# Kernel tuning notes

Measured on AMD Instinct MI355X. Metric: run time of the kernel, lower is better.

The kernel has to match this reference:

```python
import jax, jax.numpy as jnp
import numpy as np

K = 9            # kernel_size * dilation
ALPHA = 0.2      # LeakyReLU slope in GAT attention
LRELU = 0.01     # Grapher.layer1 default LeakyReLU slope
EPS_NORM = 1e-12
BN_EPS = 1e-5
NEG_INF = -9e15


def setup_inputs() -> dict:
    key = jax.random.key(0)
    ks = jax.random.split(key, 9)
    B, C, H, W = 16, 64, 32, 32
    nheads, nhid = 4, 15
    return {
        "x": jax.random.normal(ks[0], (B, C, H, W), jnp.float32),
        "W_heads": jax.random.normal(ks[1], (nheads, C, nhid), jnp.float32) * 0.2,
        "a_heads": jax.random.normal(ks[2], (nheads, 2 * nhid, 1), jnp.float32) * 0.2,
        "W_out": jax.random.normal(ks[3], (nheads * nhid, C), jnp.float32) * 0.2,
        "a_out": jax.random.normal(ks[4], (2 * C, 1), jnp.float32) * 0.2,
        "conv_w": jax.random.normal(ks[5], (C, C), jnp.float32) * 0.1,
        "conv_b": jax.random.normal(ks[6], (C,), jnp.float32) * 0.1,
        "bn_gamma": jnp.ones((C,), jnp.float32),
        "bn_beta": jnp.zeros((C,), jnp.float32),
    }


def _gat_layer(h, adj, W, a, concat):
    # h: [B,N,Fin], W: [Fin,Fout], a: [2*Fout,1]
    Wh = h @ W                                   # [B,N,Fout]
    Fout = W.shape[1]
    f1 = Wh @ a[:Fout]                           # [B,N,1]  (a . Wh_i)
    f2 = Wh @ a[Fout:]                           # [B,N,1]  (a . Wh_j)
    e = jax.nn.leaky_relu(f1 + jnp.swapaxes(f2, 1, 2), ALPHA)  # [B,N,N]
    att = jnp.where(adj > 0, e, NEG_INF)
    att = jax.nn.softmax(att, axis=1)            # torch F.softmax(dim=1)
    hp = att @ Wh                                # [B,N,Fout]
    return jax.nn.elu(hp) if concat else hp


def reference(x, W_heads, a_heads, W_out, a_out, conv_w, conv_b, bn_gamma, bn_beta):
    B, C, H, W = x.shape
    N = H * W
    res = x
    xf = x.reshape(B, C, N)                      # [B,C,N]
    # F.normalize(p=2, dim=1)
    nrm = jnp.maximum(jnp.linalg.norm(xf, axis=1, keepdims=True), EPS_NORM)
    h = jnp.swapaxes(xf / nrm, 1, 2)             # [B,N,C]
    # KNN adjacency (built under no_grad in the original)
    hs = jax.lax.stop_gradient(h)
    sq = jnp.sum(hs * hs, axis=-1, keepdims=True)        # [B,N,1]
    dist = sq - 2.0 * (hs @ jnp.swapaxes(hs, 1, 2)) + jnp.swapaxes(sq, 1, 2)
    _, idx = jax.lax.top_k(-dist, K)                      # [B,N,K]
    adj = jnp.zeros((B, N, N), x.dtype).at[
        jnp.arange(B)[:, None, None], jnp.arange(N)[None, :, None], idx
    ].set(1.0)
    # 4-head GAT (dropout is identity in eval mode)
    heads = [_gat_layer(h, adj, W_heads[i], a_heads[i], True)
             for i in range(W_heads.shape[0])]
    hcat = jnp.concatenate(heads, axis=2)        # [B,N,60]
    out = jax.nn.elu(_gat_layer(hcat, adj, W_out, a_out, False))  # [B,N,C]
    y = jnp.swapaxes(out, 1, 2).reshape(B, C, H, W)
    y = jax.nn.leaky_relu(y, LRELU)
    # 1x1 conv + BatchNorm (eval: running_mean=0, running_var=1)
    y = jnp.einsum('bchw,oc->bohw', y, conv_w) + conv_b[None, :, None, None]
    y = y / jnp.sqrt(1.0 + BN_EPS) * bn_gamma[None, :, None, None] + bn_beta[None, :, None, None]
    return y + res
```

## Files before the change

kernel.cpp:

```cpp
#include <hip/hip_runtime.h>
#include <math.h>

#define NB 16
#define NC 64
#define NN 1024
#define NK 9
#define NH 4
#define NF 15

#define OFF_HN     0
#define OFF_SQV    1048576
#define OFF_IDX    1064960
#define OFF_DEN1   1212416
#define OFF_U1     1277952
#define OFF_DEN2   1278976
#define OFF_U2     1295360
#define OFF_F11    1296384
#define OFF_F21    1361920
#define OFF_F12    1427456
#define OFF_F22    1443840
#define OFF_E1     1460224
#define OFF_E2     2050048
#define OFF_BIG    2197504
#define OFF_DIST   OFF_BIG
#define OFF_WH1    OFF_BIG
#define OFF_HCAT   3246080
#define OFF_WH2    4294656
#define OFF_YTIL   5343232
#define ZERO_BASE  OFF_DEN1
#define ZERO_LEN   83968

__device__ __forceinline__ unsigned fkey(float x){
  unsigned b = __float_as_uint(x);
  return (b & 0x80000000u) ? ~b : (b | 0x80000000u);
}
__device__ __forceinline__ float eluf(float x){ return x > 0.f ? x : expm1f(x); }

__global__ __launch_bounds__(256) void k1_norm(const float* __restrict__ x,
                                               float* __restrict__ hn, float* __restrict__ sqv,
                                               float* __restrict__ ws){
  int t = blockIdx.x*256 + threadIdx.x;
  if (t < ZERO_LEN) ws[ZERO_BASE + t] = 0.f;
  if (t >= NB*NN) return;
  int b = t >> 10, n = t & 1023;
  const float* xb = x + b*NC*NN;
  float* hb = hn + b*NC*NN;
  float s = 0.f;
  #pragma unroll
  for (int c = 0; c < NC; c++){ float v = xb[c*NN + n]; s = fmaf(v, v, s); }
  float nrm = fmaxf(sqrtf(s), 1e-12f);
  float s2 = 0.f;
  #pragma unroll
  for (int c = 0; c < NC; c++){
    float v = xb[c*NN + n] / nrm;
    hb[c*NN + n] = v;
    s2 = fmaf(v, v, s2);
  }
  sqv[t] = s2;
}

__global__ __launch_bounds__(256) void k2a_dist(const float* __restrict__ hn,
    const float* __restrict__ sqv, float* __restrict__ dist, int bbase){
  __shared__ float As[64][128];
  __shared__ float Bs[64][128];
  int b = bbase + blockIdx.y;
  int i0 = (blockIdx.x >> 3) * 128, j0 = (blockIdx.x & 7) * 128;
  const float* hb = hn + b*NC*NN;
  for (int t = threadIdx.x; t < 64*128; t += 256){
    int c = t >> 7, ii = t & 127;
    As[c][ii] = hb[c*NN + i0 + ii];
    Bs[c][ii] = hb[c*NN + j0 + ii];
  }
  __syncthreads();
  int tx = threadIdx.x & 15, ty = threadIdx.x >> 4;
  float acc[8][8];
  #pragma unroll
  for (int q = 0; q < 8; q++)
    #pragma unroll
    for (int jj = 0; jj < 8; jj++) acc[q][jj] = 0.f;
  #pragma unroll 4
  for (int c = 0; c < 64; c++){
    float4 a0 = *(const float4*)&As[c][ty*8];
    float4 a1 = *(const float4*)&As[c][ty*8+4];
    float4 b0 = *(const float4*)&Bs[c][tx*8];
    float4 b1 = *(const float4*)&Bs[c][tx*8+4];
    float av[8], bv[8];
    av[0]=a0.x; av[1]=a0.y; av[2]=a0.z; av[3]=a0.w; av[4]=a1.x; av[5]=a1.y; av[6]=a1.z; av[7]=a1.w;
    bv[0]=b0.x; bv[1]=b0.y; bv[2]=b0.z; bv[3]=b0.w; bv[4]=b1.x; bv[5]=b1.y; bv[6]=b1.z; bv[7]=b1.w;
    #pragma unroll
    for (int q = 0; q < 8; q++)
      #pragma unroll
      for (int jj = 0; jj < 8; jj++) acc[q][jj] = fmaf(av[q], bv[jj], acc[q][jj]);
  }
  const float* sv = sqv + b*NN;
  float sj[8];
  #pragma unroll
  for (int jj = 0; jj < 8; jj++) sj[jj] = sv[j0 + tx*8 + jj];
  #pragma unroll
  for (int q = 0; q < 8; q++){
    float si = sv[i0 + ty*8 + q];
    float o0[8];
    #pragma unroll
    for (int jj = 0; jj < 8; jj++) o0[jj] = (si - 2.f*acc[q][jj]) + sj[jj];
    float* dp = dist + (size_t)((blockIdx.y*NN) + i0 + ty*8 + q)*NN + j0 + tx*8;
    *(float4*)&dp[0] = make_float4(o0[0],o0[1],o0[2],o0[3]);
    *(float4*)&dp[4] = make_float4(o0[4],o0[5],o0[6],o0[7]);
  }
}

__global__ __launch_bounds__(256) void k2b_top9(const float* __restrict__ dist,
                                                int* __restrict__ idxb, int bbase){
  int wave = threadIdx.x >> 6, lane = threadIdx.x & 63;
  int rlocal = blockIdx.x*4 + wave;
  int bl = rlocal >> 10;
  int i  = rlocal & 1023;
  const float* dr = dist + (size_t)rlocal*NN;
  unsigned long long key[16];
  #pragma unroll
  for (int m = 0; m < 16; m++){
    int j = m*64 + lane;
    key[m] = ((unsigned long long)fkey(dr[j]) << 32) | (unsigned)j;
  }
  int* op = idxb + (size_t)(((bbase + bl)*NN) + i)*NK;
  for (int round = 0; round < NK; round++){
    unsigned long long best = key[0];
    #pragma unroll
    for (int m = 1; m < 16; m++) best = key[m] < best ? key[m] : best;
    #pragma unroll
    for (int off = 32; off >= 1; off >>= 1){
      unsigned long long o = __shfl_xor(best, off);
      best = o < best ? o : best;
    }
    if (lane == 0) op[round] = (int)(best & 0xFFFFFFFFu);
    int wl = (int)(best & 63u);
    int wm = (int)((best >> 6) & 15u);
    if (lane == wl) key[wm] = ~0ull;
  }
}

__global__ __launch_bounds__(256) void k3_wh1(const float* __restrict__ hn,
    const float* __restrict__ W_heads, const float* __restrict__ a_heads,
    float* __restrict__ Wh1, float* __restrict__ f1, float* __restrict__ f2){
  int b = blockIdx.y;
  int n = blockIdx.x*256 + threadIdx.x;
  const float* hb = hn + b*NC*NN;
  float wh[NH][NF];
  #pragma unroll
  for (int hh = 0; hh < NH; hh++)
    #pragma unroll
    for (int f = 0; f < NF; f++) wh[hh][f] = 0.f;
  for (int c = 0; c < NC; c++){
    float xv = hb[c*NN + n];
    #pragma unroll
    for (int hh = 0; hh < NH; hh++){
      const float* W = W_heads + (hh*NC + c)*NF;
      #pragma unroll
      for (int f = 0; f < NF; f++) wh[hh][f] = fmaf(xv, W[f], wh[hh][f]);
    }
  }
  float* orow = Wh1 + ((size_t)(b*NN) + n)*64;
  #pragma unroll
  for (int hh = 0; hh < NH; hh++){
    const float* al = a_heads + hh*2*NF;
    float s1 = 0.f, s2 = 0.f;
    #pragma unroll
    for (int f = 0; f < NF; f++){ s1 = fmaf(wh[hh][f], al[f], s1); s2 = fmaf(wh[hh][f], al[NF+f], s2); }
    float4* o4 = (float4*)(orow + hh*16);
    o4[0] = make_float4(wh[hh][0], wh[hh][1], wh[hh][2], wh[hh][3]);
    o4[1] = make_float4(wh[hh][4], wh[hh][5], wh[hh][6], wh[hh][7]);
    o4[2] = make_float4(wh[hh][8], wh[hh][9], wh[hh][10], wh[hh][11]);
    o4[3] = make_float4(wh[hh][12], wh[hh][13], wh[hh][14], 0.f);
    int hb2 = hh*NB + b;
    f1[hb2*NN + n] = s1; f2[hb2*NN + n] = s2;
  }
}

__global__ __launch_bounds__(256) void k4_edge1(const int* __restrict__ idxb, const float* __restrict__ f1,
                         const float* __restrict__ f2, float* __restrict__ e1,
                         float* __restrict__ denom1){
  int t = blockIdx.x*256 + threadIdx.x;
  int k = t % 9; int rest = t / 9; int i = rest & 1023; int hb = rest >> 10;
  int b = hb & 15;
  int j = idxb[((b*NN) + i)*NK + k];
  float e = f1[hb*NN + i] + f2[hb*NN + j];
  e = e >= 0.f ? e : 0.2f*e;
  e1[t] = e;
  atomicAdd(denom1 + hb*NN + j, expf(e));
  (void)k;
}

__global__ __launch_bounds__(256) void k4b_u1(const float* __restrict__ denom1,
                       const float* __restrict__ Wh1, float* __restrict__ u1){
  int t = blockIdx.x*256 + threadIdx.x;
  if (denom1[t] != 0.f) return;
  int hb = t >> 10, j = t & 1023;
  int hh = hb >> 4, b = hb & 15;
  const float* w = Wh1 + ((size_t)(b*NN) + j)*64 + hh*16;
  for (int f = 0; f < NF; f++) atomicAdd(u1 + hb*16 + f, w[f] * (1.f/1024.f));
}

__global__ __launch_bounds__(256) void k5_hp1(const int* __restrict__ idxb, const float* __restrict__ e1,
    const float* __restrict__ denom1, const float* __restrict__ Wh1,
    const float* __restrict__ u1, float* __restrict__ hcat){
  int wave = threadIdx.x >> 6, lane = threadIdx.x & 63;
  int t = blockIdx.x*4 + wave;
  int b = t >> 10, i = t & 1023;
  int hh = lane >> 4, f = lane & 15;
  int hb = hh*NB + b;
  float acc = u1[hb*16 + f];
  const int* jp = idxb + (size_t)t*NK;
  const float* ep = e1 + (size_t)(hb*NN + i)*NK;
  const float* dn = denom1 + hb*NN;
  const float* wbase = Wh1 + ((size_t)(b*NN))*64;
  #pragma unroll 3
  for (int k = 0; k < NK; k++){
    int j = jp[k];
    float att = expf(ep[k]) / dn[j];
    acc = fmaf(att, wbase[(size_t)j*64 + lane], acc);
  }
  if (f < NF) hcat[((size_t)(b*NN) + i)*64 + hh*NF + f] = eluf(acc);
}

__global__ __launch_bounds__(256) void k7_wh2(const float* __restrict__ hcat,
    const float* __restrict__ W_out, const float* __restrict__ a_out,
    float* __restrict__ Wh2, float* __restrict__ f1, float* __restrict__ f2){
  __shared__ float hcl[64][65];
  __shared__ float p1[4][64], p2[4][64];
  int b = blockIdx.y, n0 = blockIdx.x*64;
  for (int t = threadIdx.x; t < 4096; t += 256){
    int nl = t >> 6, c = t & 63;
    hcl[nl][c] = hcat[(size_t)((b*NN) + n0 + nl)*64 + c];
  }
  __syncthreads();
  int nl = threadIdx.x & 63;
  int wv = threadIdx.x >> 6;
  int og = __builtin_amdgcn_readfirstlane(wv * 16);
  float z[16];
  #pragma unroll
  for (int m = 0; m < 16; m++) z[m] = 0.f;
  for (int c = 0; c < 60; c++){
    float yv = hcl[nl][c];
    #pragma unroll
    for (int m = 0; m < 16; m++) z[m] = fmaf(yv, W_out[c*64 + og + m], z[m]);
  }
  int n = n0 + nl;
  float* o = Wh2 + ((size_t)(b*NN) + n)*64 + og;
  #pragma unroll
  for (int m = 0; m < 16; m += 4) *(float4*)&o[m] = make_float4(z[m],z[m+1],z[m+2],z[m+3]);
  float s1 = 0.f, s2 = 0.f;
  #pragma unroll
  for (int m = 0; m < 16; m++){ s1 = fmaf(z[m], a_out[og+m], s1); s2 = fmaf(z[m], a_out[64+og+m], s2); }
  p1[wv][nl] = s1; p2[wv][nl] = s2;
  __syncthreads();
  if (threadIdx.x < 64){
    f1[b*NN + n0 + threadIdx.x] = p1[0][threadIdx.x] + p1[1][threadIdx.x] + p1[2][threadIdx.x] + p1[3][threadIdx.x];
    f2[b*NN + n0 + threadIdx.x] = p2[0][threadIdx.x] + p2[1][threadIdx.x] + p2[2][threadIdx.x] + p2[3][threadIdx.x];
  }
}

__global__ __launch_bounds__(256) void k8_edge2(const int* __restrict__ idxb, const float* __restrict__ f1,
                         const float* __restrict__ f2, float* __restrict__ e2,
                         float* __restrict__ denom2){
  int t = blockIdx.x*256 + threadIdx.x;
  int bi = t / 9;
  int b = bi >> 10;
  int j = idxb[t];
  float e = f1[bi] + f2[b*NN + j];
  e = e >= 0.f ? e : 0.2f*e;
  e2[t] = e;
  atomicAdd(denom2 + b*NN + j, expf(e));
}

__global__ __launch_bounds__(256) void k8b_u2(const float* __restrict__ denom2,
                       const float* __restrict__ Wh2, float* __restrict__ u2){
  int t = blockIdx.x*256 + threadIdx.x;
  if (denom2[t] != 0.f) return;
  int b = t >> 10;
  const float* w = Wh2 + (size_t)t*64;
  for (int f = 0; f < 64; f++) atomicAdd(u2 + b*64 + f, w[f] * (1.f/1024.f));
}

__global__ __launch_bounds__(256) void k9_hp2(const int* __restrict__ idxb, const float* __restrict__ e2,
    const float* __restrict__ denom2, const float* __restrict__ Wh2,
    const float* __restrict__ u2, float* __restrict__ ytil){
  int wave = threadIdx.x >> 6, lane = threadIdx.x & 63;
  int t = blockIdx.x*4 + wave;
  int b = t >> 10;
  float acc = u2[b*64 + lane];
  const int* jp = idxb + (size_t)t*NK;
  const float* ep = e2 + (size_t)t*NK;
  const float* dn = denom2 + b*NN;
  const float* wbase = Wh2 + ((size_t)(b*NN))*64;
  #pragma unroll 3
  for (int k = 0; k < NK; k++){
    int j = jp[k];
    float att = expf(ep[k]) / dn[j];
    acc = fmaf(att, wbase[(size_t)j*64 + lane], acc);
  }
  float v = eluf(acc);
  ytil[(size_t)t*64 + lane] = v >= 0.f ? v : 0.01f*v;
}

__global__ __launch_bounds__(256) void k11_conv(const float* __restrict__ ytil,
    const float* __restrict__ conv_w, const float* __restrict__ conv_b,
    const float* __restrict__ bn_g, const float* __restrict__ bn_b,
    const float* __restrict__ x, float* __restrict__ out){
  __shared__ float yt[64][65];
  int b = blockIdx.y, n0 = blockIdx.x*64;
  for (int t = threadIdx.x; t < 4096; t += 256){
    int nl = t >> 6, c = t & 63;
    yt[nl][c] = ytil[(size_t)((b*NN) + n0 + nl)*64 + c];
  }
  __syncthreads();
  int nl = threadIdx.x & 63;
  int og = __builtin_amdgcn_readfirstlane((int)(threadIdx.x >> 6) * 16);
  float z[16];
  #pragma unroll
  for (int m = 0; m < 16; m++) z[m] = 0.f;
  for (int c = 0; c < 64; c++){
    float yv = yt[nl][c];
    #pragma unroll
    for (int m = 0; m < 16; m++) z[m] = fmaf(yv, conv_w[(og+m)*64 + c], z[m]);
  }
  const float scbn = 1.f / sqrtf(1.f + 1e-5f);
  #pragma unroll
  for (int m = 0; m < 16; m++){
    int o = og + m;
    size_t oi = ((size_t)(b*64 + o))*NN + n0 + nl;
    out[oi] = fmaf(z[m] + conv_b[o], bn_g[o]*scbn, bn_b[o]) + x[oi];
  }
}

extern "C" void kernel_launch(void* const* d_in, const int* in_sizes, int n_in,
                              void* d_out, int out_size, void* d_ws, size_t ws_size,
                              hipStream_t stream){
  (void)in_sizes; (void)n_in; (void)out_size; (void)ws_size;
  const float* x       = (const float*)d_in[0];
  const float* W_heads = (const float*)d_in[1];
  const float* a_heads = (const float*)d_in[2];
  const float* W_out   = (const float*)d_in[3];
  const float* a_out   = (const float*)d_in[4];
  const float* conv_w  = (const float*)d_in[5];
  const float* conv_b  = (const float*)d_in[6];
  const float* bn_g    = (const float*)d_in[7];
  const float* bn_b    = (const float*)d_in[8];
  float* ws  = (float*)d_ws;
  float* out = (float*)d_out;

  float* hn   = ws + OFF_HN;
  float* sqv  = ws + OFF_SQV;
  int*   idxb = (int*)(ws + OFF_IDX);
  float* den1 = ws + OFF_DEN1;
  float* u1   = ws + OFF_U1;
  float* den2 = ws + OFF_DEN2;
  float* u2   = ws + OFF_U2;
  float* f11  = ws + OFF_F11;
  float* f21  = ws + OFF_F21;
  float* f12  = ws + OFF_F12;
  float* f22  = ws + OFF_F22;
  float* e1   = ws + OFF_E1;
  float* e2   = ws + OFF_E2;
  float* Wh1  = ws + OFF_WH1;
  float* hcat = ws + OFF_HCAT;
  float* Wh2  = ws + OFF_WH2;
  float* ytil = ws + OFF_YTIL;
  float* dist = ws + OFF_DIST;

  k1_norm<<<dim3(328), dim3(256), 0, stream>>>(x, hn, sqv, ws);
  for (int bb = 0; bb < NB; bb += 4){
    k2a_dist<<<dim3(64,4), dim3(256), 0, stream>>>(hn, sqv, dist, bb);
    k2b_top9<<<dim3(1024), dim3(256), 0, stream>>>(dist, idxb, bb);
  }
  k3_wh1<<<dim3(4,16), dim3(256), 0, stream>>>(hn, W_heads, a_heads, Wh1, f11, f21);
  k4_edge1<<<dim3(2304), dim3(256), 0, stream>>>(idxb, f11, f21, e1, den1);
  k4b_u1<<<dim3(256), dim3(256), 0, stream>>>(den1, Wh1, u1);
  k5_hp1<<<dim3(4096), dim3(256), 0, stream>>>(idxb, e1, den1, Wh1, u1, hcat);
  k7_wh2<<<dim3(16,16), dim3(256), 0, stream>>>(hcat, W_out, a_out, Wh2, f12, f22);
  k8_edge2<<<dim3(576), dim3(256), 0, stream>>>(idxb, f12, f22, e2, den2);
  k8b_u2<<<dim3(64), dim3(256), 0, stream>>>(den2, Wh2, u2);
  k9_hp2<<<dim3(4096), dim3(256), 0, stream>>>(idxb, e2, den2, Wh2, u2, ytil);
  k11_conv<<<dim3(16,16), dim3(256), 0, stream>>>(ytil, conv_w, conv_b, bn_g, bn_b, x, out);
}
```

Before: 315.0 us.

## Fuse head projection into normalization and edge scores into top-k selection

The layer-1 head projection (Wh1, f1, f2) is folded into the normalization kernel, so the normalized features are consumed directly instead of being re-read by a separate kernel. The per-edge attention logits and denominator atomics are computed inside the top-9 kernel from indices kept in shared memory. The distance matrix gets its own buffer for all 16 batches, so the four batched dist/top-k launch pairs collapse into one launch each. This cuts kernel launches and intermediate traffic, but needs a much larger workspace (a full 16-batch distance matrix) and makes the normalization kernel heavier in registers.

After: 270.3 us. -14.2%, faster.

```diff
diff --git a/kernel.cpp b/kernel.cpp
--- a/kernel.cpp
+++ b/kernel.cpp
@@ -21,12 +21,11 @@
 #define OFF_F22    1443840
 #define OFF_E1     1460224
 #define OFF_E2     2050048
-#define OFF_BIG    2197504
-#define OFF_DIST   OFF_BIG
-#define OFF_WH1    OFF_BIG
+#define OFF_WH1    2197504
 #define OFF_HCAT   3246080
 #define OFF_WH2    4294656
 #define OFF_YTIL   5343232
+#define OFF_DIST   6391808
 #define ZERO_BASE  OFF_DEN1
 #define ZERO_LEN   83968
 
@@ -36,9 +35,10 @@
 }
 __device__ __forceinline__ float eluf(float x){ return x > 0.f ? x : expm1f(x); }
 
-__global__ __launch_bounds__(256) void k1_norm(const float* __restrict__ x,
-                                               float* __restrict__ hn, float* __restrict__ sqv,
-                                               float* __restrict__ ws){
+__global__ __launch_bounds__(256) void k1_norm_wh(const float* __restrict__ x,
+    const float* __restrict__ W_heads, const float* __restrict__ a_heads,
+    float* __restrict__ hn, float* __restrict__ sqv, float* __restrict__ Wh1,
+    float* __restrict__ f1, float* __restrict__ f2, float* __restrict__ ws){
   int t = blockIdx.x*256 + threadIdx.x;
   if (t < ZERO_LEN) ws[ZERO_BASE + t] = 0.f;
   if (t >= NB*NN) return;
@@ -49,21 +49,46 @@
   #pragma unroll
   for (int c = 0; c < NC; c++){ float v = xb[c*NN + n]; s = fmaf(v, v, s); }
   float nrm = fmaxf(sqrtf(s), 1e-12f);
+  float wh[NH][NF];
+  #pragma unroll
+  for (int hh = 0; hh < NH; hh++)
+    #pragma unroll
+    for (int f = 0; f < NF; f++) wh[hh][f] = 0.f;
   float s2 = 0.f;
-  #pragma unroll
   for (int c = 0; c < NC; c++){
     float v = xb[c*NN + n] / nrm;
     hb[c*NN + n] = v;
     s2 = fmaf(v, v, s2);
+    #pragma unroll
+    for (int hh = 0; hh < NH; hh++){
+      const float* W = W_heads + (hh*NC + c)*NF;
+      #pragma unroll
+      for (int f = 0; f < NF; f++) wh[hh][f] = fmaf(v, W[f], wh[hh][f]);
+    }
   }
   sqv[t] = s2;
+  float* orow = Wh1 + ((size_t)(b*NN) + n)*64;
+  #pragma unroll
+  for (int hh = 0; hh < NH; hh++){
+    const float* al = a_heads + hh*2*NF;
+    float s1 = 0.f, sb = 0.f;
+    #pragma unroll
+    for (int f = 0; f < NF; f++){ s1 = fmaf(wh[hh][f], al[f], s1); sb = fmaf(wh[hh][f], al[NF+f], sb); }
+    float4* o4 = (float4*)(orow + hh*16);
+    o4[0] = make_float4(wh[hh][0], wh[hh][1], wh[hh][2], wh[hh][3]);
+    o4[1] = make_float4(wh[hh][4], wh[hh][5], wh[hh][6], wh[hh][7]);
+    o4[2] = make_float4(wh[hh][8], wh[hh][9], wh[hh][10], wh[hh][11]);
+    o4[3] = make_float4(wh[hh][12], wh[hh][13], wh[hh][14], 0.f);
+    int hb2 = hh*NB + b;
+    f1[hb2*NN + n] = s1; f2[hb2*NN + n] = sb;
+  }
 }
 
 __global__ __launch_bounds__(256) void k2a_dist(const float* __restrict__ hn,
-    const float* __restrict__ sqv, float* __restrict__ dist, int bbase){
+    const float* __restrict__ sqv, float* __restrict__ dist){
   __shared__ float As[64][128];
   __shared__ float Bs[64][128];
-  int b = bbase + blockIdx.y;
+  int b = blockIdx.y;
   int i0 = (blockIdx.x >> 3) * 128, j0 = (blockIdx.x & 7) * 128;
   const float* hb = hn + b*NC*NN;
   for (int t = threadIdx.x; t < 64*128; t += 256){
@@ -102,26 +127,26 @@
     float o0[8];
     #pragma unroll
     for (int jj = 0; jj < 8; jj++) o0[jj] = (si - 2.f*acc[q][jj]) + sj[jj];
-    float* dp = dist + (size_t)((blockIdx.y*NN) + i0 + ty*8 + q)*NN + j0 + tx*8;
+    float* dp = dist + (size_t)((b*NN) + i0 + ty*8 + q)*NN + j0 + tx*8;
     *(float4*)&dp[0] = make_float4(o0[0],o0[1],o0[2],o0[3]);
     *(float4*)&dp[4] = make_float4(o0[4],o0[5],o0[6],o0[7]);
   }
 }
 
-__global__ __launch_bounds__(256) void k2b_top9(const float* __restrict__ dist,
-                                                int* __restrict__ idxb, int bbase){
+__global__ __launch_bounds__(256) void k2b_top9e(const float* __restrict__ dist,
+    int* __restrict__ idxb, const float* __restrict__ f1, const float* __restrict__ f2,
+    float* __restrict__ e1, float* __restrict__ den1){
+  __shared__ int sj[4][16];
   int wave = threadIdx.x >> 6, lane = threadIdx.x & 63;
-  int rlocal = blockIdx.x*4 + wave;
-  int bl = rlocal >> 10;
-  int i  = rlocal & 1023;
-  const float* dr = dist + (size_t)rlocal*NN;
+  int t = blockIdx.x*4 + wave;
+  int b = t >> 10, i = t & 1023;
+  const float* dr = dist + (size_t)t*NN;
   unsigned long long key[16];
   #pragma unroll
   for (int m = 0; m < 16; m++){
     int j = m*64 + lane;
     key[m] = ((unsigned long long)fkey(dr[j]) << 32) | (unsigned)j;
   }
-  int* op = idxb + (size_t)(((bbase + bl)*NN) + i)*NK;
   for (int round = 0; round < NK; round++){
     unsigned long long best = key[0];
     #pragma unroll
@@ -131,62 +156,22 @@
       unsigned long long o = __shfl_xor(best, off);
       best = o < best ? o : best;
     }
-    if (lane == 0) op[round] = (int)(best & 0xFFFFFFFFu);
+    if (lane == 0) sj[wave][round] = (int)(best & 0xFFFFFFFFu);
     int wl = (int)(best & 63u);
     int wm = (int)((best >> 6) & 15u);
     if (lane == wl) key[wm] = ~0ull;
   }
-}
-
-__global__ __launch_bounds__(256) void k3_wh1(const float* __restrict__ hn,
-    const float* __restrict__ W_heads, const float* __restrict__ a_heads,
-    float* __restrict__ Wh1, float* __restrict__ f1, float* __restrict__ f2){
-  int b = blockIdx.y;
-  int n = blockIdx.x*256 + threadIdx.x;
-  const float* hb = hn + b*NC*NN;
-  float wh[NH][NF];
-  #pragma unroll
-  for (int hh = 0; hh < NH; hh++)
-    #pragma unroll
-    for (int f = 0; f < NF; f++) wh[hh][f] = 0.f;
-  for (int c = 0; c < NC; c++){
-    float xv = hb[c*NN + n];
-    #pragma unroll
-    for (int hh = 0; hh < NH; hh++){
-      const float* W = W_heads + (hh*NC + c)*NF;
-      #pragma unroll
-      for (int f = 0; f < NF; f++) wh[hh][f] = fmaf(xv, W[f], wh[hh][f]);
-    }
-  }
-  float* orow = Wh1 + ((size_t)(b*NN) + n)*64;
-  #pragma unroll
-  for (int hh = 0; hh < NH; hh++){
-    const float* al = a_heads + hh*2*NF;
-    float s1 = 0.f, s2 = 0.f;
-    #pragma unroll
-    for (int f = 0; f < NF; f++){ s1 = fmaf(wh[hh][f], al[f], s1); s2 = fmaf(wh[hh][f], al[NF+f], s2); }
-    float4* o4 = (float4*)(orow + hh*16);
-    o4[0] = make_float4(wh[hh][0], wh[hh][1], wh[hh][2], wh[hh][3]);
-    o4[1] = make_float4(wh[hh][4], wh[hh][5], wh[hh][6], wh[hh][7]);
-    o4[2] = make_float4(wh[hh][8], wh[hh][9], wh[hh][10], wh[hh][11]);
-    o4[3] = make_float4(wh[hh][12], wh[hh][13], wh[hh][14], 0.f);
-    int hb2 = hh*NB + b;
-    f1[hb2*NN + n] = s1; f2[hb2*NN + n] = s2;
-  }
-}
-
-__global__ __launch_bounds__(256) void k4_edge1(const int* __restrict__ idxb, const float* __restrict__ f1,
-                         const float* __restrict__ f2, float* __restrict__ e1,
-                         float* __restrict__ denom1){
-  int t = blockIdx.x*256 + threadIdx.x;
-  int k = t % 9; int rest = t / 9; int i = rest & 1023; int hb = rest >> 10;
-  int b = hb & 15;
-  int j = idxb[((b*NN) + i)*NK + k];
-  float e = f1[hb*NN + i] + f2[hb*NN + j];
-  e = e >= 0.f ? e : 0.2f*e;
-  e1[t] = e;
-  atomicAdd(denom1 + hb*NN + j, expf(e));
-  (void)k;
+  __syncthreads();
+  if (lane < NK) idxb[(size_t)t*NK + lane] = sj[wave][lane];
+  if (lane < 36){
+    int k = lane >> 2, hh = lane & 3;
+    int j = sj[wave][k];
+    int hb = hh*NB + b;
+    float e = f1[hb*NN + i] + f2[hb*NN + j];
+    e = e >= 0.f ? e : 0.2f*e;
+    e1[(size_t)(hb*NN + i)*NK + k] = e;
+    atomicAdd(den1 + hb*NN + j, expf(e));
+  }
 }
 
 __global__ __launch_bounds__(256) void k4b_u1(const float* __restrict__ denom1,
@@ -366,13 +351,9 @@
   float* ytil = ws + OFF_YTIL;
   float* dist = ws + OFF_DIST;
 
-  k1_norm<<<dim3(328), dim3(256), 0, stream>>>(x, hn, sqv, ws);
-  for (int bb = 0; bb < NB; bb += 4){
-    k2a_dist<<<dim3(64,4), dim3(256), 0, stream>>>(hn, sqv, dist, bb);
-    k2b_top9<<<dim3(1024), dim3(256), 0, stream>>>(dist, idxb, bb);
-  }
-  k3_wh1<<<dim3(4,16), dim3(256), 0, stream>>>(hn, W_heads, a_heads, Wh1, f11, f21);
-  k4_edge1<<<dim3(2304), dim3(256), 0, stream>>>(idxb, f11, f21, e1, den1);
+  k1_norm_wh<<<dim3(328), dim3(256), 0, stream>>>(x, W_heads, a_heads, hn, sqv, Wh1, f11, f21, ws);
+  k2a_dist<<<dim3(64,16), dim3(256), 0, stream>>>(hn, sqv, dist);
+  k2b_top9e<<<dim3(4096), dim3(256), 0, stream>>>(dist, idxb, f11, f21, e1, den1);
   k4b_u1<<<dim3(256), dim3(256), 0, stream>>>(den1, Wh1, u1);
   k5_hp1<<<dim3(4096), dim3(256), 0, stream>>>(idxb, e1, den1, Wh1, u1, hcat);
   k7_wh2<<<dim3(16,16), dim3(256), 0, stream>>>(hcat, W_out, a_out, Wh2, f12, f22);
```
